# Performance work log

Hardware: AMD Instinct MI355X
Metric: run time of the kernel (lower is better)

The kernel has to match this reference:

```python
import jax, jax.numpy as jnp
import numpy as np

N = 320   # coalition size (number of prefix steps)
D = 512   # input_dim / attention weight_dim


def setup_inputs() -> dict:
    key = jax.random.key(0)
    ks = jax.random.split(key, 10)
    s = 1.0 / np.sqrt(D)  # torch Linear default init range
    u = lambda k, shape: jax.random.uniform(k, shape, jnp.float32, -s, s)
    return {
        "x": jax.random.normal(ks[0], (N, D), jnp.float32),
        "goal": jax.random.normal(ks[1], (D,), jnp.float32),
        "Wq": u(ks[2], (D, D)), "bq": u(ks[3], (D,)),
        "Wk": u(ks[4], (D, D)), "bk": u(ks[5], (D,)),
        "Wv": u(ks[6], (D, D)), "bv": u(ks[7], (D,)),
        # norm_col_init(std=0.1): small column-normalized weights; bias zero-filled
        "Wc": 0.01 * jax.random.normal(ks[8], (1, 2 * D), jnp.float32),
        "bc": jnp.zeros((1,), jnp.float32),
    }


def reference(x, goal, Wq, bq, Wk, bk, Wv, bv, Wc, bc):
    # x: [n, d] coalition features. goal is unused by the original forward.
    n, d = x.shape
    q = x @ Wq.T + bq  # [n, d]
    k = x @ Wk.T + bk
    v = x @ Wv.T + bv
    scores = (q @ k.T) / jnp.sqrt(jnp.asarray(d, x.dtype))  # [n, n]

    # Prefix lengths j = 1..n-1. For each j, attention over coalition[:j]:
    # softmax over keys < j (rows < j are the only valid queries), then the
    # AttentionLayer global feature = mean over query rows of attn @ v.
    j = jnp.arange(1, n)                          # [n-1]
    idx = jnp.arange(n)
    prefix_mask = idx[None, :] < j[:, None]       # [n-1, n], True for k < j
    neg = jnp.finfo(scores.dtype).min
    masked = jnp.where(prefix_mask[:, None, :], scores[None, :, :], neg)  # [n-1, n, n]
    att = jax.nn.softmax(masked, axis=-1)         # rows >= j are garbage, masked below
    # mean over valid query rows i < j, fused before multiplying by V:
    pooled = jnp.sum(att * prefix_mask[:, :, None], axis=1) / j[:, None].astype(x.dtype)  # [n-1, n]
    feats = pooled @ v                            # [n-1, d] global feature per prefix

    # j = 0 uses a zero feature vector
    features = jnp.concatenate([jnp.zeros((1, d), x.dtype), feats], axis=0)  # [n, d]
    cat = jnp.concatenate([features, x], axis=1)  # [n, 2d]
    vals = cat @ Wc.T + bc                        # [n, 1] critic outputs
    return jnp.sum(vals)[None]                    # scalar value, shape [1]
```

## Files before the change

kernel.cpp:

```cpp
#include <hip/hip_runtime.h>

#define NC 320
#define DIM 512

__global__ __launch_bounds__(256) void big1(
    const float* __restrict__ x,
    const float* __restrict__ Wq, const float* __restrict__ Wk,
    const float* __restrict__ Wv, const float* __restrict__ Wc,
    float* __restrict__ partQK,
    float* __restrict__ hpart)
{
  const int b = blockIdx.x;
  const int t = threadIdx.x;

  if (b >= 640) {
    const int d0 = (b - 640) * 32;
    for (int ei = t; ei < DIM; ei += 256) {
      float s = 0.f;
      #pragma unroll
      for (int d = 0; d < 32; ++d)
        s = fmaf(Wv[(d0 + d) * DIM + ei], Wc[d0 + d], s);
      hpart[(b - 640) * DIM + ei] = s;
    }
    return;
  }

  __shared__ __align__(16) float As[32][68];
  __shared__ __align__(16) float Bs[32][68];

  const int z   = b / 40;
  const int rem = b % 40;
  const int i0  = (rem / 8) * 64;
  const int c0  = (rem % 8) * 64;
  const float* __restrict__ W = (z & 8) ? Wk : Wq;
  const int kb = (z & 7) * 64;

  const int sr = t >> 2;
  const int kc = (t & 3) << 3;
  const int ty = t >> 4;
  const int tx = t & 15;

  float acc[4][4] = {};
  const float* xp = x + (i0 + sr) * DIM + kc;
  const float* wp = W + (c0 + sr) * DIM + kc;

  for (int k0 = kb; k0 < kb + 64; k0 += 32) {
    const float4 xa = *(const float4*)(xp + k0);
    const float4 xb = *(const float4*)(xp + k0 + 4);
    const float4 wa = *(const float4*)(wp + k0);
    const float4 wb = *(const float4*)(wp + k0 + 4);
    __syncthreads();
    As[kc+0][sr]=xa.x; As[kc+1][sr]=xa.y; As[kc+2][sr]=xa.z; As[kc+3][sr]=xa.w;
    As[kc+4][sr]=xb.x; As[kc+5][sr]=xb.y; As[kc+6][sr]=xb.z; As[kc+7][sr]=xb.w;
    Bs[kc+0][sr]=wa.x; Bs[kc+1][sr]=wa.y; Bs[kc+2][sr]=wa.z; Bs[kc+3][sr]=wa.w;
    Bs[kc+4][sr]=wb.x; Bs[kc+5][sr]=wb.y; Bs[kc+6][sr]=wb.z; Bs[kc+7][sr]=wb.w;
    __syncthreads();
    #pragma unroll
    for (int kk = 0; kk < 32; ++kk) {
      const float4 a4 = *(const float4*)&As[kk][ty * 4];
      const float4 b4 = *(const float4*)&Bs[kk][tx * 4];
      const float a[4] = {a4.x, a4.y, a4.z, a4.w};
      const float bb[4] = {b4.x, b4.y, b4.z, b4.w};
      #pragma unroll
      for (int i = 0; i < 4; ++i)
        #pragma unroll
        for (int j = 0; j < 4; ++j)
          acc[i][j] = fmaf(a[i], bb[j], acc[i][j]);
    }
  }
  float* outq = partQK + (size_t)z * NC * DIM;
  #pragma unroll
  for (int i = 0; i < 4; ++i) {
    float4 o = {acc[i][0], acc[i][1], acc[i][2], acc[i][3]};
    *(float4*)&outq[(i0 + ty*4 + i) * DIM + c0 + tx*4] = o;
  }
}

__global__ __launch_bounds__(256) void reduce_qk(
    const float* __restrict__ part,
    const float* __restrict__ bq, const float* __restrict__ bk,
    float* __restrict__ q, float* __restrict__ k)
{
  const int mat = blockIdx.y;
  const int f   = blockIdx.x * 256 + threadIdx.x;
  const int row = f >> 7;
  const int col = (f & 127) * 4;
  const float* bias = mat ? bk : bq;
  float4 s = *(const float4*)&bias[col];
  const size_t off = (size_t)row * DIM + col;
  #pragma unroll
  for (int sp = 0; sp < 8; ++sp) {
    const float4 p = *(const float4*)&part[(size_t)(mat*8+sp) * NC * DIM + off];
    s.x += p.x; s.y += p.y; s.z += p.z; s.w += p.w;
  }
  float* out = mat ? k : q;
  *(float4*)&out[off] = s;
}

__global__ __launch_bounds__(256) void scores_u(
    const float* __restrict__ qbuf, const float* __restrict__ kbuf,
    const float* __restrict__ x,    const float* __restrict__ hpart,
    const float* __restrict__ bv,   const float* __restrict__ Wc,
    const float* __restrict__ bc,
    float* __restrict__ partS,
    float* __restrict__ u, float* __restrict__ out)
{
  const int b    = blockIdx.x;
  const int t    = threadIdx.x;
  const int lane = t & 63;
  const int wave = t >> 6;

  if (b >= 200) {
    __shared__ float red[12];
    const int r = b - 200;

    float cp = bv[t] * Wc[t] + bv[t + 256] * Wc[t + 256];
    float su = 0.f, sw = 0.f;
    for (int ei = t; ei < DIM; ei += 256) {
      float hs = 0.f;
      #pragma unroll
      for (int sp = 0; sp < 16; ++sp) hs += hpart[sp * DIM + ei];
      const float xv = x[r * DIM + ei];
      su = fmaf(xv, hs, su);
      sw = fmaf(xv, Wc[DIM + ei], sw);
    }
    #pragma unroll
    for (int off = 32; off; off >>= 1) {
      cp += __shfl_down(cp, off);
      su += __shfl_down(su, off);
      sw += __shfl_down(sw, off);
    }
    if (lane == 0) { red[wave] = cp; red[4 + wave] = su; red[8 + wave] = sw; }
    __syncthreads();
    if (t == 0) {
      const float c  = red[0] + red[1] + red[2] + red[3];
      const float sU = red[4] + red[5] + red[6] + red[7];
      float sW = red[8] + red[9] + red[10] + red[11];
      u[r] = sU + c;
      if (r == 0) sW += (float)NC * bc[0];
      atomicAdd(out, sW);
    }
    return;
  }

  __shared__ __align__(16) float As[32][68];
  __shared__ __align__(16) float Bs[32][68];

  const int z   = b / 25;
  const int rem = b % 25;
  const int i0  = (rem / 5) * 64;
  const int j0  = (rem % 5) * 64;
  const int kb  = z * 64;

  const int sr = t >> 2;
  const int kc = (t & 3) << 3;
  const int ty = t >> 4;
  const int tx = t & 15;

  float acc[4][4] = {};
  const float* qp = qbuf + (i0 + sr) * DIM + kc;
  const float* kp = kbuf + (j0 + sr) * DIM + kc;

  for (int k0 = kb; k0 < kb + 64; k0 += 32) {
    const float4 qa  = *(const float4*)(qp + k0);
    const float4 qb2 = *(const float4*)(qp + k0 + 4);
    const float4 ka  = *(const float4*)(kp + k0);
    const float4 kb4 = *(const float4*)(kp + k0 + 4);
    __syncthreads();
    As[kc+0][sr]=qa.x;  As[kc+1][sr]=qa.y;  As[kc+2][sr]=qa.z;  As[kc+3][sr]=qa.w;
    As[kc+4][sr]=qb2.x; As[kc+5][sr]=qb2.y; As[kc+6][sr]=qb2.z; As[kc+7][sr]=qb2.w;
    Bs[kc+0][sr]=ka.x;  Bs[kc+1][sr]=ka.y;  Bs[kc+2][sr]=ka.z;  Bs[kc+3][sr]=ka.w;
    Bs[kc+4][sr]=kb4.x; Bs[kc+5][sr]=kb4.y; Bs[kc+6][sr]=kb4.z; Bs[kc+7][sr]=kb4.w;
    __syncthreads();
    #pragma unroll
    for (int kk = 0; kk < 32; ++kk) {
      const float4 a4 = *(const float4*)&As[kk][ty * 4];
      const float4 b4 = *(const float4*)&Bs[kk][tx * 4];
      const float a[4] = {a4.x, a4.y, a4.z, a4.w};
      const float bb[4] = {b4.x, b4.y, b4.z, b4.w};
      #pragma unroll
      for (int i = 0; i < 4; ++i)
        #pragma unroll
        for (int j = 0; j < 4; ++j)
          acc[i][j] = fmaf(a[i], bb[j], acc[i][j]);
    }
  }
  float* outs = partS + (size_t)z * NC * NC;
  #pragma unroll
  for (int i = 0; i < 4; ++i) {
    float4 o = {acc[i][0], acc[i][1], acc[i][2], acc[i][3]};
    *(float4*)&outs[(i0 + ty*4 + i) * NC + j0 + tx*4] = o;
  }
}

__global__ __launch_bounds__(256) void row_ops3(
    const float* __restrict__ partS, const float* __restrict__ u,
    float* __restrict__ out)
{
  const int i    = blockIdx.x;
  const int t    = threadIdx.x;
  const int lane = t & 63;
  const int wave = t >> 6;

  __shared__ float e[NC];
  __shared__ float Warr[NC];
  __shared__ float Csuf[NC + 1];
  __shared__ float wred[4];

  const float scale = 0.044194173824159216f;
  for (int kk = t; kk < NC; kk += 256) {
    float s = 0.f;
    #pragma unroll
    for (int sp = 0; sp < 8; ++sp)
      s += partS[(size_t)sp * NC * NC + i * NC + kk];
    e[kk] = s * scale;
  }
  __syncthreads();

  float m = -1e30f;
  for (int kk = t; kk < NC; kk += 256) m = fmaxf(m, e[kk]);
  #pragma unroll
  for (int off = 32; off; off >>= 1) m = fmaxf(m, __shfl_down(m, off));
  if (lane == 0) wred[wave] = m;
  __syncthreads();
  m = fmaxf(fmaxf(wred[0], wred[1]), fmaxf(wred[2], wred[3]));

  for (int kk = t; kk < NC; kk += 256) e[kk] = __expf(e[kk] - m);
  __syncthreads();

  if (wave == 0) {
    float carry = 0.f;
    #pragma unroll
    for (int c = 0; c < 5; ++c) {
      const int idx = c * 64 + lane;
      float val = e[idx];
      #pragma unroll
      for (int off = 1; off < 64; off <<= 1) {
        const float nv = __shfl_up(val, off);
        if (lane >= off) val += nv;
      }
      const float incl = val + carry;
      const int j = idx + 1;
      if (j < NC) Warr[j] = (j > i) ? 1.f / ((float)j * incl) : 0.f;
      carry += __shfl(val, 63);
    }
    if (lane == 0) Warr[0] = 0.f;

    carry = 0.f;
    #pragma unroll
    for (int c = 4; c >= 0; --c) {
      const int idx = c * 64 + lane;
      float val = Warr[idx];
      #pragma unroll
      for (int off = 1; off < 64; off <<= 1) {
        const float nv = __shfl_down(val, off);
        if (lane + off < 64) val += nv;
      }
      Csuf[idx] = val + carry;
      carry += __shfl(val, 0);
    }
    if (lane == 0) Csuf[NC] = 0.f;
  }
  __syncthreads();

  float acc = 0.f;
  for (int kk = t; kk < NC; kk += 256) {
    const int mm = (i > kk) ? i : kk;
    acc += e[kk] * Csuf[mm + 1] * u[kk];
  }
  #pragma unroll
  for (int off = 32; off; off >>= 1) acc += __shfl_down(acc, off);
  __syncthreads();
  if (lane == 0) wred[wave] = acc;
  __syncthreads();
  if (t == 0)
    atomicAdd(out, wred[0] + wred[1] + wred[2] + wred[3]);
}

extern "C" void kernel_launch(void* const* d_in, const int* in_sizes, int n_in,
                              void* d_out, int out_size, void* d_ws, size_t ws_size,
                              hipStream_t stream) {
  const float* x  = (const float*)d_in[0];
  const float* Wq = (const float*)d_in[2];
  const float* bq = (const float*)d_in[3];
  const float* Wk = (const float*)d_in[4];
  const float* bk = (const float*)d_in[5];
  const float* Wv = (const float*)d_in[6];
  const float* bv = (const float*)d_in[7];
  const float* Wc = (const float*)d_in[8];
  const float* bc = (const float*)d_in[9];

  float* ws     = (float*)d_ws;
  float* partQK = ws;
  float* partS  = partQK + 16 * NC * DIM;
  float* qbuf   = partS + 8 * NC * NC;
  float* kbuf   = qbuf + NC * DIM;
  float* hpart  = kbuf + NC * DIM;
  float* u      = hpart + 16 * DIM;
  float* out    = (float*)d_out;

  hipMemsetAsync(out, 0, sizeof(float), stream);

  big1<<<656, 256, 0, stream>>>(x, Wq, Wk, Wv, Wc, partQK, hpart);
  reduce_qk<<<dim3(160, 2), 256, 0, stream>>>(partQK, bq, bk, qbuf, kbuf);
  scores_u<<<520, 256, 0, stream>>>(qbuf, kbuf, x, hpart, bv, Wc, bc,
                                    partS, u, out);
  row_ops3<<<NC, 256, 0, stream>>>(partS, u, out);
}
```

Baseline: 104.8 us.

## Fuse four launches into one cooperative kernel with grid syncs

Replaces the memset plus four separate kernel launches with a single cooperative kernel that runs each former stage in turn, separated by grid.sync barriers. Output zeroing moves into the kernel. The aim is to remove per-launch overhead and inter-kernel gaps, which matter at this small size. The cost is that grid-wide barriers hold idle blocks, and 656 blocks must all be resident at once. The old multi-kernel path stays as a fallback if the cooperative launch fails.

```diff
diff --git a/kernel.cpp b/kernel.cpp
--- a/kernel.cpp
+++ b/kernel.cpp
@@ -1,14 +1,279 @@
 #include <hip/hip_runtime.h>
+#include <hip/hip_cooperative_groups.h>
+
+namespace cg = cooperative_groups;
 
 #define NC 320
 #define DIM 512
+
+__global__ __launch_bounds__(256, 3) void fused_all(
+    const float* __restrict__ x,
+    const float* __restrict__ Wq, const float* __restrict__ bq,
+    const float* __restrict__ Wk, const float* __restrict__ bk,
+    const float* __restrict__ Wv, const float* __restrict__ bv,
+    const float* __restrict__ Wc, const float* __restrict__ bc,
+    float* __restrict__ partQK,
+    float* __restrict__ partS,
+    float* __restrict__ qbuf, float* __restrict__ kbuf,
+    float* __restrict__ hpart,
+    float* __restrict__ u,
+    float* __restrict__ out)
+{
+  cg::grid_group grid = cg::this_grid();
+
+  const int b    = blockIdx.x;
+  const int t    = threadIdx.x;
+  const int lane = t & 63;
+  const int wave = t >> 6;
+
+  __shared__ __align__(16) float As[32][68];
+  __shared__ __align__(16) float Bs[32][68];
+  __shared__ float e[NC];
+  __shared__ float Warr[NC];
+  __shared__ float Csuf[NC + 1];
+  __shared__ float wred[12];
+
+  if (b == 0 && t == 0) out[0] = 0.f;
+
+  if (b >= 640) {
+    const int d0 = (b - 640) * 32;
+    for (int ei = t; ei < DIM; ei += 256) {
+      float s = 0.f;
+      #pragma unroll
+      for (int d = 0; d < 32; ++d)
+        s = fmaf(Wv[(d0 + d) * DIM + ei], Wc[d0 + d], s);
+      hpart[(b - 640) * DIM + ei] = s;
+    }
+  } else {
+    const int z   = b / 40;
+    const int rem = b % 40;
+    const int i0  = (rem / 8) * 64;
+    const int c0  = (rem % 8) * 64;
+    const float* __restrict__ W = (z & 8) ? Wk : Wq;
+    const int kb = (z & 7) * 64;
+
+    const int sr = t >> 2;
+    const int kc = (t & 3) << 3;
+    const int ty = t >> 4;
+    const int tx = t & 15;
+
+    float acc[4][4] = {};
+    const float* xp = x + (i0 + sr) * DIM + kc;
+    const float* wp = W + (c0 + sr) * DIM + kc;
+
+    for (int k0 = kb; k0 < kb + 64; k0 += 32) {
+      const float4 xa = *(const float4*)(xp + k0);
+      const float4 xb = *(const float4*)(xp + k0 + 4);
+      const float4 wa = *(const float4*)(wp + k0);
+      const float4 wb = *(const float4*)(wp + k0 + 4);
+      __syncthreads();
+      As[kc+0][sr]=xa.x; As[kc+1][sr]=xa.y; As[kc+2][sr]=xa.z; As[kc+3][sr]=xa.w;
+      As[kc+4][sr]=xb.x; As[kc+5][sr]=xb.y; As[kc+6][sr]=xb.z; As[kc+7][sr]=xb.w;
+      Bs[kc+0][sr]=wa.x; Bs[kc+1][sr]=wa.y; Bs[kc+2][sr]=wa.z; Bs[kc+3][sr]=wa.w;
+      Bs[kc+4][sr]=wb.x; Bs[kc+5][sr]=wb.y; Bs[kc+6][sr]=wb.z; Bs[kc+7][sr]=wb.w;
+      __syncthreads();
+      #pragma unroll
+      for (int kk = 0; kk < 32; ++kk) {
+        const float4 a4 = *(const float4*)&As[kk][ty * 4];
+        const float4 b4 = *(const float4*)&Bs[kk][tx * 4];
+        const float a[4] = {a4.x, a4.y, a4.z, a4.w};
+        const float bb[4] = {b4.x, b4.y, b4.z, b4.w};
+        #pragma unroll
+        for (int i = 0; i < 4; ++i)
+          #pragma unroll
+          for (int j = 0; j < 4; ++j)
+            acc[i][j] = fmaf(a[i], bb[j], acc[i][j]);
+      }
+    }
+    float* outq = partQK + (size_t)z * NC * DIM;
+    #pragma unroll
+    for (int i = 0; i < 4; ++i) {
+      float4 o = {acc[i][0], acc[i][1], acc[i][2], acc[i][3]};
+      *(float4*)&outq[(i0 + ty*4 + i) * DIM + c0 + tx*4] = o;
+    }
+  }
+
+  grid.sync();
+
+  if (b < 320) {
+    const int mat = b / 160;
+    const int f   = (b % 160) * 256 + t;
+    const int row = f >> 7;
+    const int col = (f & 127) * 4;
+    const float* bias = mat ? bk : bq;
+    float4 s = *(const float4*)&bias[col];
+    const size_t off = (size_t)row * DIM + col;
+    #pragma unroll
+    for (int sp = 0; sp < 8; ++sp) {
+      const float4 p = *(const float4*)&partQK[(size_t)(mat*8+sp) * NC * DIM + off];
+      s.x += p.x; s.y += p.y; s.z += p.z; s.w += p.w;
+    }
+    float* o = mat ? kbuf : qbuf;
+    *(float4*)&o[off] = s;
+  }
+
+  grid.sync();
+
+  if (b < 520) {
+    if (b >= 200) {
+      const int r = b - 200;
+
+      float cp = bv[t] * Wc[t] + bv[t + 256] * Wc[t + 256];
+      float su = 0.f, sw = 0.f;
+      for (int ei = t; ei < DIM; ei += 256) {
+        float hs = 0.f;
+        #pragma unroll
+        for (int sp = 0; sp < 16; ++sp) hs += hpart[sp * DIM + ei];
+        const float xv = x[r * DIM + ei];
+        su = fmaf(xv, hs, su);
+        sw = fmaf(xv, Wc[DIM + ei], sw);
+      }
+      #pragma unroll
+      for (int off = 32; off; off >>= 1) {
+        cp += __shfl_down(cp, off);
+        su += __shfl_down(su, off);
+        sw += __shfl_down(sw, off);
+      }
+      if (lane == 0) { wred[wave] = cp; wred[4 + wave] = su; wred[8 + wave] = sw; }
+      __syncthreads();
+      if (t == 0) {
+        const float c  = wred[0] + wred[1] + wred[2] + wred[3];
+        const float sU = wred[4] + wred[5] + wred[6] + wred[7];
+        float sW = wred[8] + wred[9] + wred[10] + wred[11];
+        u[r] = sU + c;
+        if (r == 0) sW += (float)NC * bc[0];
+        atomicAdd(out, sW);
+      }
+    } else {
+      const int z   = b / 25;
+      const int rem = b % 25;
+      const int i0  = (rem / 5) * 64;
+      const int j0  = (rem % 5) * 64;
+      const int kb  = z * 64;
+
+      const int sr = t >> 2;
+      const int kc = (t & 3) << 3;
+      const int ty = t >> 4;
+      const int tx = t & 15;
+
+      float acc[4][4] = {};
+      const float* qp = qbuf + (i0 + sr) * DIM + kc;
+      const float* kp = kbuf + (j0 + sr) * DIM + kc;
+
+      for (int k0 = kb; k0 < kb + 64; k0 += 32) {
+        const float4 qa  = *(const float4*)(qp + k0);
+        const float4 qb2 = *(const float4*)(qp + k0 + 4);
+        const float4 ka  = *(const float4*)(kp + k0);
+        const float4 kb4 = *(const float4*)(kp + k0 + 4);
+        __syncthreads();
+        As[kc+0][sr]=qa.x;  As[kc+1][sr]=qa.y;  As[kc+2][sr]=qa.z;  As[kc+3][sr]=qa.w;
+        As[kc+4][sr]=qb2.x; As[kc+5][sr]=qb2.y; As[kc+6][sr]=qb2.z; As[kc+7][sr]=qb2.w;
+        Bs[kc+0][sr]=ka.x;  Bs[kc+1][sr]=ka.y;  Bs[kc+2][sr]=ka.z;  Bs[kc+3][sr]=ka.w;
+        Bs[kc+4][sr]=kb4.x; Bs[kc+5][sr]=kb4.y; Bs[kc+6][sr]=kb4.z; Bs[kc+7][sr]=kb4.w;
+        __syncthreads();
+        #pragma unroll
+        for (int kk = 0; kk < 32; ++kk) {
+          const float4 a4 = *(const float4*)&As[kk][ty * 4];
+          const float4 b4 = *(const float4*)&Bs[kk][tx * 4];
+          const float a[4] = {a4.x, a4.y, a4.z, a4.w};
+          const float bb[4] = {b4.x, b4.y, b4.z, b4.w};
+          #pragma unroll
+          for (int i = 0; i < 4; ++i)
+            #pragma unroll
+            for (int j = 0; j < 4; ++j)
+              acc[i][j] = fmaf(a[i], bb[j], acc[i][j]);
+        }
+      }
+      float* outs = partS + (size_t)z * NC * NC;
+      #pragma unroll
+      for (int i = 0; i < 4; ++i) {
+        float4 o = {acc[i][0], acc[i][1], acc[i][2], acc[i][3]};
+        *(float4*)&outs[(i0 + ty*4 + i) * NC + j0 + tx*4] = o;
+      }
+    }
+  }
+
+  grid.sync();
+
+  if (b < 320) {
+    const int i = b;
+
+    const float scale = 0.044194173824159216f;
+    for (int kk = t; kk < NC; kk += 256) {
+      float s = 0.f;
+      #pragma unroll
+      for (int sp = 0; sp < 8; ++sp)
+        s += partS[(size_t)sp * NC * NC + i * NC + kk];
+      e[kk] = s * scale;
+    }
+    __syncthreads();
+
+    float m = -1e30f;
+    for (int kk = t; kk < NC; kk += 256) m = fmaxf(m, e[kk]);
+    #pragma unroll
+    for (int off = 32; off; off >>= 1) m = fmaxf(m, __shfl_down(m, off));
+    if (lane == 0) wred[wave] = m;
+    __syncthreads();
+    m = fmaxf(fmaxf(wred[0], wred[1]), fmaxf(wred[2], wred[3]));
+
+    for (int kk = t; kk < NC; kk += 256) e[kk] = __expf(e[kk] - m);
+    __syncthreads();
+
+    if (wave == 0) {
+      float carry = 0.f;
+      #pragma unroll
+      for (int c = 0; c < 5; ++c) {
+        const int idx = c * 64 + lane;
+        float val = e[idx];
+        #pragma unroll
+        for (int off = 1; off < 64; off <<= 1) {
+          const float nv = __shfl_up(val, off);
+          if (lane >= off) val += nv;
+        }
+        const float incl = val + carry;
+        const int j = idx + 1;
+        if (j < NC) Warr[j] = (j > i) ? 1.f / ((float)j * incl) : 0.f;
+        carry += __shfl(val, 63);
+      }
+      if (lane == 0) Warr[0] = 0.f;
+
+      carry = 0.f;
+      #pragma unroll
+      for (int c = 4; c >= 0; --c) {
+        const int idx = c * 64 + lane;
+        float val = Warr[idx];
+        #pragma unroll
+        for (int off = 1; off < 64; off <<= 1) {
+          const float nv = __shfl_down(val, off);
+          if (lane + off < 64) val += nv;
+        }
+        Csuf[idx] = val + carry;
+        carry += __shfl(val, 0);
+      }
+      if (lane == 0) Csuf[NC] = 0.f;
+    }
+    __syncthreads();
+
+    float acc = 0.f;
+    for (int kk = t; kk < NC; kk += 256) {
+      const int mm = (i > kk) ? i : kk;
+      acc += e[kk] * Csuf[mm + 1] * u[kk];
+    }
+    #pragma unroll
+    for (int off = 32; off; off >>= 1) acc += __shfl_down(acc, off);
+    __syncthreads();
+    if (lane == 0) wred[wave] = acc;
+    __syncthreads();
+    if (t == 0)
+      atomicAdd(out, wred[0] + wred[1] + wred[2] + wred[3]);
+  }
+}
 
 __global__ __launch_bounds__(256) void big1(
     const float* __restrict__ x,
     const float* __restrict__ Wq, const float* __restrict__ Wk,
     const float* __restrict__ Wv, const float* __restrict__ Wc,
-    float* __restrict__ partQK,
-    float* __restrict__ hpart)
+    float* __restrict__ partQK, float* __restrict__ hpart)
 {
   const int b = blockIdx.x;
   const int t = threadIdx.x;
@@ -299,11 +564,23 @@
   float* u      = hpart + 16 * DIM;
   float* out    = (float*)d_out;
 
-  hipMemsetAsync(out, 0, sizeof(float), stream);
-
-  big1<<<656, 256, 0, stream>>>(x, Wq, Wk, Wv, Wc, partQK, hpart);
-  reduce_qk<<<dim3(160, 2), 256, 0, stream>>>(partQK, bq, bk, qbuf, kbuf);
-  scores_u<<<520, 256, 0, stream>>>(qbuf, kbuf, x, hpart, bv, Wc, bc,
-                                    partS, u, out);
-  row_ops3<<<NC, 256, 0, stream>>>(partS, u, out);
+  void* args[] = {
+    (void*)&x,
+    (void*)&Wq, (void*)&bq, (void*)&Wk, (void*)&bk,
+    (void*)&Wv, (void*)&bv, (void*)&Wc, (void*)&bc,
+    (void*)&partQK, (void*)&partS, (void*)&qbuf, (void*)&kbuf,
+    (void*)&hpart, (void*)&u, (void*)&out
+  };
+
+  hipError_t err = hipLaunchCooperativeKernel(
+      (const void*)fused_all, dim3(656), dim3(256), args, 0, stream);
+
+  if (err != hipSuccess) {
+    hipMemsetAsync(out, 0, sizeof(float), stream);
+    big1<<<656, 256, 0, stream>>>(x, Wq, Wk, Wv, Wc, partQK, hpart);
+    reduce_qk<<<dim3(160, 2), 256, 0, stream>>>(partQK, bq, bk, qbuf, kbuf);
+    scores_u<<<520, 256, 0, stream>>>(qbuf, kbuf, x, hpart, bv, Wc, bc,
+                                      partS, u, out);
+    row_ops3<<<NC, 256, 0, stream>>>(partS, u, out);
+  }
 }
```

After: 352.5 us. +236.5%, slower.

## Fuse score GEMM into row softmax kernel and drop memset launch

Applied to the files above, without the earlier changes.

Removes the split-K score GEMM and its partial buffer. Each block of 320 threads now computes two query rows of scores directly against K, each thread handling one key row, then runs the softmax, prefix-scan and weighting in shared memory. The u computation moves into the bias-reduction kernel, and zeroing the output moves into the first kernel instead of a memset, cutting the chain from four launches plus a memset to three launches. The cost is only 160 blocks with strided, uncoalesced per-thread reads of K rows, which may use the GPU less well than the old tiled GEMM.

```diff
diff --git a/kernel.cpp b/kernel.cpp
--- a/kernel.cpp
+++ b/kernel.cpp
@@ -8,10 +8,13 @@
     const float* __restrict__ Wq, const float* __restrict__ Wk,
     const float* __restrict__ Wv, const float* __restrict__ Wc,
     float* __restrict__ partQK,
-    float* __restrict__ hpart)
+    float* __restrict__ hpart,
+    float* __restrict__ out)
 {
   const int b = blockIdx.x;
   const int t = threadIdx.x;
+
+  if (b == 0 && t == 0) out[0] = 0.f;
 
   if (b >= 640) {
     const int d0 = (b - 640) * 32;
@@ -76,205 +79,196 @@
   }
 }
 
-__global__ __launch_bounds__(256) void reduce_qk(
-    const float* __restrict__ part,
+__global__ __launch_bounds__(256) void reduce_qk_u(
+    const float* __restrict__ partQK,
     const float* __restrict__ bq, const float* __restrict__ bk,
-    float* __restrict__ q, float* __restrict__ k)
-{
-  const int mat = blockIdx.y;
-  const int f   = blockIdx.x * 256 + threadIdx.x;
-  const int row = f >> 7;
-  const int col = (f & 127) * 4;
-  const float* bias = mat ? bk : bq;
-  float4 s = *(const float4*)&bias[col];
-  const size_t off = (size_t)row * DIM + col;
-  #pragma unroll
-  for (int sp = 0; sp < 8; ++sp) {
-    const float4 p = *(const float4*)&part[(size_t)(mat*8+sp) * NC * DIM + off];
-    s.x += p.x; s.y += p.y; s.z += p.z; s.w += p.w;
-  }
-  float* out = mat ? k : q;
-  *(float4*)&out[off] = s;
-}
-
-__global__ __launch_bounds__(256) void scores_u(
-    const float* __restrict__ qbuf, const float* __restrict__ kbuf,
-    const float* __restrict__ x,    const float* __restrict__ hpart,
-    const float* __restrict__ bv,   const float* __restrict__ Wc,
+    const float* __restrict__ x,  const float* __restrict__ hpart,
+    const float* __restrict__ bv, const float* __restrict__ Wc,
     const float* __restrict__ bc,
-    float* __restrict__ partS,
+    float* __restrict__ q, float* __restrict__ k,
     float* __restrict__ u, float* __restrict__ out)
 {
-  const int b    = blockIdx.x;
+  const int b = blockIdx.x;
+  const int t = threadIdx.x;
+
+  if (b < 320) {
+    const int mat = b / 160;
+    const int f   = (b % 160) * 256 + t;
+    const int row = f >> 7;
+    const int col = (f & 127) * 4;
+    const float* bias = mat ? bk : bq;
+    float4 s = *(const float4*)&bias[col];
+    const size_t off = (size_t)row * DIM + col;
+    #pragma unroll
+    for (int sp = 0; sp < 8; ++sp) {
+      const float4 p = *(const float4*)&partQK[(size_t)(mat*8+sp) * NC * DIM + off];
+      s.x += p.x; s.y += p.y; s.z += p.z; s.w += p.w;
+    }
+    float* o = mat ? k : q;
+    *(float4*)&o[off] = s;
+    return;
+  }
+
+  __shared__ float red[12];
+  const int lane = t & 63;
+  const int wave = t >> 6;
+  const int r = b - 320;
+
+  float cp = bv[t] * Wc[t] + bv[t + 256] * Wc[t + 256];
+  float su = 0.f, sw = 0.f;
+  for (int ei = t; ei < DIM; ei += 256) {
+    float hs = 0.f;
+    #pragma unroll
+    for (int sp = 0; sp < 16; ++sp) hs += hpart[sp * DIM + ei];
+    const float xv = x[r * DIM + ei];
+    su = fmaf(xv, hs, su);
+    sw = fmaf(xv, Wc[DIM + ei], sw);
+  }
+  #pragma unroll
+  for (int off = 32; off; off >>= 1) {
+    cp += __shfl_down(cp, off);
+    su += __shfl_down(su, off);
+    sw += __shfl_down(sw, off);
+  }
+  if (lane == 0) { red[wave] = cp; red[4 + wave] = su; red[8 + wave] = sw; }
+  __syncthreads();
+  if (t == 0) {
+    const float c  = red[0] + red[1] + red[2] + red[3];
+    const float sU = red[4] + red[5] + red[6] + red[7];
+    float sW = red[8] + red[9] + red[10] + red[11];
+    u[r] = sU + c;
+    if (r == 0) sW += (float)NC * bc[0];
+    atomicAdd(out, sW);
+  }
+}
+
+__global__ __launch_bounds__(320) void rows_fused(
+    const float* __restrict__ qbuf, const float* __restrict__ kbuf,
+    const float* __restrict__ u, float* __restrict__ out)
+{
+  const int bi   = blockIdx.x;
   const int t    = threadIdx.x;
   const int lane = t & 63;
   const int wave = t >> 6;
 
-  if (b >= 200) {
-    __shared__ float red[12];
-    const int r = b - 200;
-
-    float cp = bv[t] * Wc[t] + bv[t + 256] * Wc[t + 256];
-    float su = 0.f, sw = 0.f;
-    for (int ei = t; ei < DIM; ei += 256) {
-      float hs = 0.f;
-      #pragma unroll
-      for (int sp = 0; sp < 16; ++sp) hs += hpart[sp * DIM + ei];
-      const float xv = x[r * DIM + ei];
-      su = fmaf(xv, hs, su);
-      sw = fmaf(xv, Wc[DIM + ei], sw);
-    }
-    #pragma unroll
-    for (int off = 32; off; off >>= 1) {
-      cp += __shfl_down(cp, off);
-      su += __shfl_down(su, off);
-      sw += __shfl_down(sw, off);
-    }
-    if (lane == 0) { red[wave] = cp; red[4 + wave] = su; red[8 + wave] = sw; }
-    __syncthreads();
-    if (t == 0) {
-      const float c  = red[0] + red[1] + red[2] + red[3];
-      const float sU = red[4] + red[5] + red[6] + red[7];
-      float sW = red[8] + red[9] + red[10] + red[11];
-      u[r] = sU + c;
-      if (r == 0) sW += (float)NC * bc[0];
-      atomicAdd(out, sW);
-    }
-    return;
-  }
-
-  __shared__ __align__(16) float As[32][68];
-  __shared__ __align__(16) float Bs[32][68];
-
-  const int z   = b / 25;
-  const int rem = b % 25;
-  const int i0  = (rem / 5) * 64;
-  const int j0  = (rem % 5) * 64;
-  const int kb  = z * 64;
-
-  const int sr = t >> 2;
-  const int kc = (t & 3) << 3;
-  const int ty = t >> 4;
-  const int tx = t & 15;
-
-  float acc[4][4] = {};
-  const float* qp = qbuf + (i0 + sr) * DIM + kc;
-  const float* kp = kbuf + (j0 + sr) * DIM + kc;
-
-  for (int k0 = kb; k0 < kb + 64; k0 += 32) {
-    const float4 qa  = *(const float4*)(qp + k0);
-    const float4 qb2 = *(const float4*)(qp + k0 + 4);
-    const float4 ka  = *(const float4*)(kp + k0);
-    const float4 kb4 = *(const float4*)(kp + k0 + 4);
-    __syncthreads();
-    As[kc+0][sr]=qa.x;  As[kc+1][sr]=qa.y;  As[kc+2][sr]=qa.z;  As[kc+3][sr]=qa.w;
-    As[kc+4][sr]=qb2.x; As[kc+5][sr]=qb2.y; As[kc+6][sr]=qb2.z; As[kc+7][sr]=qb2.w;
-    Bs[kc+0][sr]=ka.x;  Bs[kc+1][sr]=ka.y;  Bs[kc+2][sr]=ka.z;  Bs[kc+3][sr]=ka.w;
-    Bs[kc+4][sr]=kb4.x; Bs[kc+5][sr]=kb4.y; Bs[kc+6][sr]=kb4.z; Bs[kc+7][sr]=kb4.w;
-    __syncthreads();
-    #pragma unroll
-    for (int kk = 0; kk < 32; ++kk) {
-      const float4 a4 = *(const float4*)&As[kk][ty * 4];
-      const float4 b4 = *(const float4*)&Bs[kk][tx * 4];
-      const float a[4] = {a4.x, a4.y, a4.z, a4.w};
-      const float bb[4] = {b4.x, b4.y, b4.z, b4.w};
-      #pragma unroll
-      for (int i = 0; i < 4; ++i)
-        #pragma unroll
-        for (int j = 0; j < 4; ++j)
-          acc[i][j] = fmaf(a[i], bb[j], acc[i][j]);
-    }
-  }
-  float* outs = partS + (size_t)z * NC * NC;
-  #pragma unroll
-  for (int i = 0; i < 4; ++i) {
-    float4 o = {acc[i][0], acc[i][1], acc[i][2], acc[i][3]};
-    *(float4*)&outs[(i0 + ty*4 + i) * NC + j0 + tx*4] = o;
-  }
-}
-
-__global__ __launch_bounds__(256) void row_ops3(
-    const float* __restrict__ partS, const float* __restrict__ u,
-    float* __restrict__ out)
-{
-  const int i    = blockIdx.x;
-  const int t    = threadIdx.x;
-  const int lane = t & 63;
-  const int wave = t >> 6;
-
-  __shared__ float e[NC];
+  const int iA = bi;
+  const int iB = bi + 160;
+
+  __shared__ __align__(16) float qA[DIM];
+  __shared__ __align__(16) float qB[DIM];
+  __shared__ float eA[NC];
+  __shared__ float eB[NC];
   __shared__ float Warr[NC];
   __shared__ float Csuf[NC + 1];
   __shared__ float wred[4];
 
-  const float scale = 0.044194173824159216f;
-  for (int kk = t; kk < NC; kk += 256) {
-    float s = 0.f;
-    #pragma unroll
-    for (int sp = 0; sp < 8; ++sp)
-      s += partS[(size_t)sp * NC * NC + i * NC + kk];
-    e[kk] = s * scale;
+  for (int ei = t; ei < DIM; ei += 320) {
+    qA[ei] = qbuf[iA * DIM + ei];
+    qB[ei] = qbuf[iB * DIM + ei];
   }
   __syncthreads();
 
-  float m = -1e30f;
-  for (int kk = t; kk < NC; kk += 256) m = fmaxf(m, e[kk]);
-  #pragma unroll
-  for (int off = 32; off; off >>= 1) m = fmaxf(m, __shfl_down(m, off));
-  if (lane == 0) wred[wave] = m;
+  {
+    const float* kj = kbuf + (size_t)t * DIM;
+    float sa[8], sb[8];
+    #pragma unroll
+    for (int z = 0; z < 8; ++z) {
+      float a = 0.f, bacc = 0.f;
+      #pragma unroll
+      for (int dd = 0; dd < 64; dd += 4) {
+        const int d = z * 64 + dd;
+        const float4 kv  = *(const float4*)(kj + d);
+        const float4 qa4 = *(const float4*)&qA[d];
+        const float4 qb4 = *(const float4*)&qB[d];
+        a    = fmaf(qa4.x, kv.x, a);
+        a    = fmaf(qa4.y, kv.y, a);
+        a    = fmaf(qa4.z, kv.z, a);
+        a    = fmaf(qa4.w, kv.w, a);
+        bacc = fmaf(qb4.x, kv.x, bacc);
+        bacc = fmaf(qb4.y, kv.y, bacc);
+        bacc = fmaf(qb4.z, kv.z, bacc);
+        bacc = fmaf(qb4.w, kv.w, bacc);
+      }
+      sa[z] = a; sb[z] = bacc;
+    }
+    const float scale = 0.044194173824159216f;
+    float sA = sa[0], sB = sb[0];
+    #pragma unroll
+    for (int z = 1; z < 8; ++z) { sA += sa[z]; sB += sb[z]; }
+    eA[t] = sA * scale;
+    eB[t] = sB * scale;
+  }
   __syncthreads();
-  m = fmaxf(fmaxf(wred[0], wred[1]), fmaxf(wred[2], wred[3]));
-
-  for (int kk = t; kk < NC; kk += 256) e[kk] = __expf(e[kk] - m);
-  __syncthreads();
-
-  if (wave == 0) {
-    float carry = 0.f;
-    #pragma unroll
-    for (int c = 0; c < 5; ++c) {
-      const int idx = c * 64 + lane;
-      float val = e[idx];
-      #pragma unroll
-      for (int off = 1; off < 64; off <<= 1) {
-        const float nv = __shfl_up(val, off);
-        if (lane >= off) val += nv;
-      }
-      const float incl = val + carry;
-      const int j = idx + 1;
-      if (j < NC) Warr[j] = (j > i) ? 1.f / ((float)j * incl) : 0.f;
-      carry += __shfl(val, 63);
-    }
-    if (lane == 0) Warr[0] = 0.f;
-
-    carry = 0.f;
-    #pragma unroll
-    for (int c = 4; c >= 0; --c) {
-      const int idx = c * 64 + lane;
-      float val = Warr[idx];
-      #pragma unroll
-      for (int off = 1; off < 64; off <<= 1) {
-        const float nv = __shfl_down(val, off);
-        if (lane + off < 64) val += nv;
-      }
-      Csuf[idx] = val + carry;
-      carry += __shfl(val, 0);
-    }
-    if (lane == 0) Csuf[NC] = 0.f;
-  }
-  __syncthreads();
-
-  float acc = 0.f;
-  for (int kk = t; kk < NC; kk += 256) {
-    const int mm = (i > kk) ? i : kk;
-    acc += e[kk] * Csuf[mm + 1] * u[kk];
-  }
-  #pragma unroll
-  for (int off = 32; off; off >>= 1) acc += __shfl_down(acc, off);
-  __syncthreads();
-  if (lane == 0) wred[wave] = acc;
-  __syncthreads();
-  if (t == 0)
-    atomicAdd(out, wred[0] + wred[1] + wred[2] + wred[3]);
+
+  for (int rsel = 0; rsel < 2; ++rsel) {
+    float* e    = rsel ? eB : eA;
+    const int i = rsel ? iB : iA;
+
+    float m = -1e30f;
+    if (t < 256) {
+      for (int kk = t; kk < NC; kk += 256) m = fmaxf(m, e[kk]);
+      #pragma unroll
+      for (int off = 32; off; off >>= 1) m = fmaxf(m, __shfl_down(m, off));
+      if (lane == 0) wred[wave] = m;
+    }
+    __syncthreads();
+    m = fmaxf(fmaxf(wred[0], wred[1]), fmaxf(wred[2], wred[3]));
+
+    if (t < 256)
+      for (int kk = t; kk < NC; kk += 256) e[kk] = __expf(e[kk] - m);
+    __syncthreads();
+
+    if (wave == 0) {
+      float carry = 0.f;
+      #pragma unroll
+      for (int c = 0; c < 5; ++c) {
+        const int idx = c * 64 + lane;
+        float val = e[idx];
+        #pragma unroll
+        for (int off = 1; off < 64; off <<= 1) {
+          const float nv = __shfl_up(val, off);
+          if (lane >= off) val += nv;
+        }
+        const float incl = val + carry;
+        const int j = idx + 1;
+        if (j < NC) Warr[j] = (j > i) ? 1.f / ((float)j * incl) : 0.f;
+        carry += __shfl(val, 63);
+      }
+      if (lane == 0) Warr[0] = 0.f;
+
+      carry = 0.f;
+      #pragma unroll
+      for (int c = 4; c >= 0; --c) {
+        const int idx = c * 64 + lane;
+        float val = Warr[idx];
+        #pragma unroll
+        for (int off = 1; off < 64; off <<= 1) {
+          const float nv = __shfl_down(val, off);
+          if (lane + off < 64) val += nv;
+        }
+        Csuf[idx] = val + carry;
+        carry += __shfl(val, 0);
+      }
+      if (lane == 0) Csuf[NC] = 0.f;
+    }
+    __syncthreads();
+
+    float acc = 0.f;
+    if (t < 256) {
+      for (int kk = t; kk < NC; kk += 256) {
+        const int mm = (i > kk) ? i : kk;
+        acc += e[kk] * Csuf[mm + 1] * u[kk];
+      }
+      #pragma unroll
+      for (int off = 32; off; off >>= 1) acc += __shfl_down(acc, off);
+    }
+    __syncthreads();
+    if (t < 256 && lane == 0) wred[wave] = acc;
+    __syncthreads();
+    if (t == 0)
+      atomicAdd(out, wred[0] + wred[1] + wred[2] + wred[3]);
+    __syncthreads();
+  }
 }
 
 extern "C" void kernel_launch(void* const* d_in, const int* in_sizes, int n_in,
@@ -292,18 +286,14 @@
 
   float* ws     = (float*)d_ws;
   float* partQK = ws;
-  float* partS  = partQK + 16 * NC * DIM;
-  float* qbuf   = partS + 8 * NC * NC;
+  float* qbuf   = partQK + 16 * NC * DIM;
   float* kbuf   = qbuf + NC * DIM;
   float* hpart  = kbuf + NC * DIM;
   float* u      = hpart + 16 * DIM;
   float* out    = (float*)d_out;
 
-  hipMemsetAsync(out, 0, sizeof(float), stream);
-
-  big1<<<656, 256, 0, stream>>>(x, Wq, Wk, Wv, Wc, partQK, hpart);
-  reduce_qk<<<dim3(160, 2), 256, 0, stream>>>(partQK, bq, bk, qbuf, kbuf);
-  scores_u<<<520, 256, 0, stream>>>(qbuf, kbuf, x, hpart, bv, Wc, bc,
-                                    partS, u, out);
-  row_ops3<<<NC, 256, 0, stream>>>(partS, u, out);
-}
+  big1<<<656, 256, 0, stream>>>(x, Wq, Wk, Wv, Wc, partQK, hpart, out);
+  reduce_qk_u<<<640, 256, 0, stream>>>(partQK, bq, bk, x, hpart, bv, Wc, bc,
+                                       qbuf, kbuf, u, out);
+  rows_fused<<<160, 320, 0, stream>>>(qbuf, kbuf, u, out);
+}
```

Result: slower. 119.6 us (+14.2%).

## Drop memset and move u computation into the QK reduction kernel

Applied to the files above, without the earlier changes.

Replaces the hipMemsetAsync on the output with a store from the first thread of the first GEMM kernel. The per-row u/critic-dot blocks move out of the scores kernel into the bias-add reduction kernel, leaving a plain 200-block scores GEMM. This removes one launch and rebalances the work between kernels. The output zeroing by block 0 is only safe because the later atomicAdds come in subsequent kernels on the same stream.

```diff
diff --git a/kernel.cpp b/kernel.cpp
--- a/kernel.cpp
+++ b/kernel.cpp
@@ -8,10 +8,13 @@
     const float* __restrict__ Wq, const float* __restrict__ Wk,
     const float* __restrict__ Wv, const float* __restrict__ Wc,
     float* __restrict__ partQK,
-    float* __restrict__ hpart)
+    float* __restrict__ hpart,
+    float* __restrict__ out)
 {
   const int b = blockIdx.x;
   const int t = threadIdx.x;
+
+  if (b == 0 && t == 0) out[0] = 0.f;
 
   if (b >= 640) {
     const int d0 = (b - 640) * 32;
@@ -76,72 +79,75 @@
   }
 }
 
-__global__ __launch_bounds__(256) void reduce_qk(
-    const float* __restrict__ part,
+__global__ __launch_bounds__(256) void reduce_qk_u(
+    const float* __restrict__ partQK,
     const float* __restrict__ bq, const float* __restrict__ bk,
-    float* __restrict__ q, float* __restrict__ k)
-{
-  const int mat = blockIdx.y;
-  const int f   = blockIdx.x * 256 + threadIdx.x;
-  const int row = f >> 7;
-  const int col = (f & 127) * 4;
-  const float* bias = mat ? bk : bq;
-  float4 s = *(const float4*)&bias[col];
-  const size_t off = (size_t)row * DIM + col;
-  #pragma unroll
-  for (int sp = 0; sp < 8; ++sp) {
-    const float4 p = *(const float4*)&part[(size_t)(mat*8+sp) * NC * DIM + off];
-    s.x += p.x; s.y += p.y; s.z += p.z; s.w += p.w;
-  }
-  float* out = mat ? k : q;
-  *(float4*)&out[off] = s;
-}
-
-__global__ __launch_bounds__(256) void scores_u(
-    const float* __restrict__ qbuf, const float* __restrict__ kbuf,
-    const float* __restrict__ x,    const float* __restrict__ hpart,
-    const float* __restrict__ bv,   const float* __restrict__ Wc,
+    const float* __restrict__ x,  const float* __restrict__ hpart,
+    const float* __restrict__ bv, const float* __restrict__ Wc,
     const float* __restrict__ bc,
-    float* __restrict__ partS,
+    float* __restrict__ q, float* __restrict__ k,
     float* __restrict__ u, float* __restrict__ out)
 {
-  const int b    = blockIdx.x;
-  const int t    = threadIdx.x;
+  const int b = blockIdx.x;
+  const int t = threadIdx.x;
+
+  if (b < 320) {
+    const int mat = b / 160;
+    const int f   = (b % 160) * 256 + t;
+    const int row = f >> 7;
+    const int col = (f & 127) * 4;
+    const float* bias = mat ? bk : bq;
+    float4 s = *(const float4*)&bias[col];
+    const size_t off = (size_t)row * DIM + col;
+    #pragma unroll
+    for (int sp = 0; sp < 8; ++sp) {
+      const float4 p = *(const float4*)&partQK[(size_t)(mat*8+sp) * NC * DIM + off];
+      s.x += p.x; s.y += p.y; s.z += p.z; s.w += p.w;
+    }
+    float* o = mat ? k : q;
+    *(float4*)&o[off] = s;
+    return;
+  }
+
+  __shared__ float red[12];
   const int lane = t & 63;
   const int wave = t >> 6;
-
-  if (b >= 200) {
-    __shared__ float red[12];
-    const int r = b - 200;
-
-    float cp = bv[t] * Wc[t] + bv[t + 256] * Wc[t + 256];
-    float su = 0.f, sw = 0.f;
-    for (int ei = t; ei < DIM; ei += 256) {
-      float hs = 0.f;
-      #pragma unroll
-      for (int sp = 0; sp < 16; ++sp) hs += hpart[sp * DIM + ei];
-      const float xv = x[r * DIM + ei];
-      su = fmaf(xv, hs, su);
-      sw = fmaf(xv, Wc[DIM + ei], sw);
-    }
-    #pragma unroll
-    for (int off = 32; off; off >>= 1) {
-      cp += __shfl_down(cp, off);
-      su += __shfl_down(su, off);
-      sw += __shfl_down(sw, off);
-    }
-    if (lane == 0) { red[wave] = cp; red[4 + wave] = su; red[8 + wave] = sw; }
-    __syncthreads();
-    if (t == 0) {
-      const float c  = red[0] + red[1] + red[2] + red[3];
-      const float sU = red[4] + red[5] + red[6] + red[7];
-      float sW = red[8] + red[9] + red[10] + red[11];
-      u[r] = sU + c;
-      if (r == 0) sW += (float)NC * bc[0];
-      atomicAdd(out, sW);
-    }
-    return;
-  }
+  const int r = b - 320;
+
+  float cp = bv[t] * Wc[t] + bv[t + 256] * Wc[t + 256];
+  float su = 0.f, sw = 0.f;
+  for (int ei = t; ei < DIM; ei += 256) {
+    float hs = 0.f;
+    #pragma unroll
+    for (int sp = 0; sp < 16; ++sp) hs += hpart[sp * DIM + ei];
+    const float xv = x[r * DIM + ei];
+    su = fmaf(xv, hs, su);
+    sw = fmaf(xv, Wc[DIM + ei], sw);
+  }
+  #pragma unroll
+  for (int off = 32; off; off >>= 1) {
+    cp += __shfl_down(cp, off);
+    su += __shfl_down(su, off);
+    sw += __shfl_down(sw, off);
+  }
+  if (lane == 0) { red[wave] = cp; red[4 + wave] = su; red[8 + wave] = sw; }
+  __syncthreads();
+  if (t == 0) {
+    const float c  = red[0] + red[1] + red[2] + red[3];
+    const float sU = red[4] + red[5] + red[6] + red[7];
+    float sW = red[8] + red[9] + red[10] + red[11];
+    u[r] = sU + c;
+    if (r == 0) sW += (float)NC * bc[0];
+    atomicAdd(out, sW);
+  }
+}
+
+__global__ __launch_bounds__(256) void scores(
+    const float* __restrict__ qbuf, const float* __restrict__ kbuf,
+    float* __restrict__ partS)
+{
+  const int b = blockIdx.x;
+  const int t = threadIdx.x;
 
   __shared__ __align__(16) float As[32][68];
   __shared__ __align__(16) float Bs[32][68];
@@ -299,11 +305,9 @@
   float* u      = hpart + 16 * DIM;
   float* out    = (float*)d_out;
 
-  hipMemsetAsync(out, 0, sizeof(float), stream);
-
-  big1<<<656, 256, 0, stream>>>(x, Wq, Wk, Wv, Wc, partQK, hpart);
-  reduce_qk<<<dim3(160, 2), 256, 0, stream>>>(partQK, bq, bk, qbuf, kbuf);
-  scores_u<<<520, 256, 0, stream>>>(qbuf, kbuf, x, hpart, bv, Wc, bc,
-                                    partS, u, out);
+  big1<<<656, 256, 0, stream>>>(x, Wq, Wk, Wv, Wc, partQK, hpart, out);
+  reduce_qk_u<<<640, 256, 0, stream>>>(partQK, bq, bk, x, hpart, bv, Wc, bc,
+                                       qbuf, kbuf, u, out);
+  scores<<<200, 256, 0, stream>>>(qbuf, kbuf, partS);
   row_ops3<<<NC, 256, 0, stream>>>(partS, u, out);
 }
```

Result: no change. 105.3 us (+0.5%).
